# Optimization experiments

Measured on AMD Instinct MI355X. Metric: run time of the kernel, lower is better.

## Reference

```python
import jax, jax.numpy as jnp
import numpy as np

EPS = 1e-7
B, F, C, H, W, D = 2, 2, 64, 32, 104, 96


def _pix_homog(h, w):
    ys, xs = jnp.meshgrid(jnp.arange(h, dtype=jnp.float32),
                          jnp.arange(w, dtype=jnp.float32), indexing='ij')
    return jnp.stack([xs.ravel(), ys.ravel(), jnp.ones(h * w, jnp.float32)], 0)  # [3, H*W]


def setup_inputs() -> dict:
    key = jax.random.key(0)
    k1, k2 = jax.random.split(key)
    current_feats = jax.random.normal(k1, (B, C, H, W), jnp.float32)
    lookup_feats = jax.random.normal(k2, (B, F, C, H, W), jnp.float32)

    rng = np.random.RandomState(0)
    # intrinsics at matching (feature) resolution, monodepth2-style
    Km = np.eye(4, dtype=np.float32)
    Km[0, 0] = 0.58 * W
    Km[1, 1] = 1.92 * H
    Km[0, 2] = 0.5 * W
    Km[1, 2] = 0.5 * H
    K = np.tile(Km[None], (B, 1, 1))
    invK = np.linalg.inv(K).astype(np.float32)

    # near-identity relative poses (small rotation perturbation + small translation)
    poses = np.tile(np.eye(4, dtype=np.float32)[None, None], (B, F, 1, 1))
    poses[:, :, :3, :3] += 0.02 * rng.randn(B, F, 3, 3).astype(np.float32)
    poses[:, :, :3, 3] = 0.1 * rng.randn(B, F, 3).astype(np.float32)

    depth_bins = jnp.linspace(0.1, 20.0, D, dtype=jnp.float32)
    return {
        'current_feats': current_feats,
        'lookup_feats': lookup_feats,
        'poses': jnp.asarray(poses),
        'K': jnp.asarray(K),
        'invK': jnp.asarray(invK),
        'depth_bins': depth_bins,
    }


def _grid_sample_zeros(lfT, gx, gy, h, w):
    """Bilinear grid_sample, align_corners=True, padding_mode='zeros'.
    lfT: [B,F,H,W,C]; gx,gy: [B,F,D,H,W] in pixel coords. -> [B,F,D,H,W,C]"""
    x0 = jnp.floor(gx)
    y0 = jnp.floor(gy)
    x0i = x0.astype(jnp.int32)
    y0i = y0.astype(jnp.int32)
    wx1 = gx - x0
    wy1 = gy - y0
    wx0 = 1.0 - wx1
    wy0 = 1.0 - wy1
    bb = jnp.arange(lfT.shape[0])[:, None, None, None, None]
    ff = jnp.arange(lfT.shape[1])[None, :, None, None, None]

    def corner(yi, xi, wgt):
        m = ((xi >= 0) & (xi < w) & (yi >= 0) & (yi < h)).astype(lfT.dtype)
        xc = jnp.clip(xi, 0, w - 1)
        yc = jnp.clip(yi, 0, h - 1)
        v = lfT[bb, ff, yc, xc]                      # [B,F,D,H,W,C]
        return v * (m * wgt)[..., None]

    return (corner(y0i, x0i, wy0 * wx0) + corner(y0i, x0i + 1, wy0 * wx1)
            + corner(y0i + 1, x0i, wy1 * wx0) + corner(y0i + 1, x0i + 1, wy1 * wx1))


def reference(current_feats, lookup_feats, poses, K, invK, depth_bins):
    b, c, h, w = current_feats.shape
    f = lookup_feats.shape[1]
    d = depth_bins.shape[0]

    # Backproject: world points for each hypothesised depth plane
    pix = _pix_homog(h, w)                                   # [3, HW]
    cam = jnp.einsum('bij,jn->bin', invK[:, :3, :3], pix)    # [B,3,HW]
    pts = depth_bins[None, :, None, None] * cam[:, None]     # [B,D,3,HW]
    world = jnp.concatenate([pts, jnp.ones((b, d, 1, h * w), pts.dtype)], 2)  # [B,D,4,HW]

    # Project into each lookup frame
    P = jnp.einsum('bij,bfjk->bfik', K, poses)[:, :, :3, :]  # [B,F,3,4]
    cpts = jnp.einsum('bfij,bdjn->bfdin', P, world)          # [B,F,D,3,HW]
    xy = cpts[:, :, :, :2] / (cpts[:, :, :, 2:3] + EPS)      # pixel coords [B,F,D,2,HW]
    xy = xy.reshape(b, f, d, 2, h, w)
    gx, gy = xy[:, :, :, 0], xy[:, :, :, 1]                  # [B,F,D,H,W]

    # edge mask (detach in original -> stop_gradient)
    sx, sy = jax.lax.stop_gradient(gx), jax.lax.stop_gradient(gy)
    edge = ((sx >= 2.0) & (sx <= w - 2) & (sy >= 2.0) & (sy <= h - 2)).astype(jnp.float32)
    interior = jnp.zeros((h, w), jnp.float32).at[2:-2, 2:-2].set(1.0)
    edge_mask = edge * interior                               # [B,F,D,H,W]

    # warp lookup features and L1-diff against current features
    lfT = lookup_feats.transpose(0, 1, 3, 4, 2)               # [B,F,H,W,C]
    warped = _grid_sample_zeros(lfT, gx, gy, h, w)            # [B,F,D,H,W,C]
    cur = current_feats.transpose(0, 2, 3, 1)                 # [B,H,W,C]
    diffs = jnp.abs(warped - cur[:, None, None]).mean(-1) * edge_mask  # [B,F,D,H,W]

    # skip lookup frames whose pose is all-zero
    valid = (poses.sum((-2, -1)) != 0).astype(jnp.float32)    # [B,F]
    diffs = diffs * valid[:, :, None, None, None]

    cost = diffs.sum(1)                                        # [B,D,H,W]
    counts = (diffs > 0).astype(jnp.float32).sum(1)
    cost = cost / (counts + EPS)

    # set missing values to per-pixel max over depth bins
    missing = (cost == 0.0)
    cmax = cost.max(1, keepdims=True)
    cost = jnp.where(missing, cmax, cost)
    return cost
```

## Files before the change

### kernel.cpp

```cpp
#include <hip/hip_runtime.h>
#include <math.h>

constexpr int B_ = 2, F_ = 2, C_ = 64, H_ = 32, W_ = 104, D_ = 96;
constexpr int HW_ = H_ * W_;
#define EPSF 1e-7f

constexpr size_t LFP_ELEMS  = (size_t)B_ * F_ * HW_ * C_;
constexpr size_t CURT_OFF_F = LFP_ELEMS;

constexpr int NT_BLKS = (HW_ / 32) * (C_ / 32) * (B_ * F_ + B_);
constexpr int PXB   = 4;
constexpr int XT_   = W_ / PXB;
constexpr int DPAD  = D_ + 1;
constexpr int DPADI = D_ + 4;


template<int CTRL>
__device__ __forceinline__ float dpp_add(float x) {
    int y = __builtin_amdgcn_update_dpp(0, __float_as_int(x), CTRL, 0xf, 0xf, true);
    return x + __int_as_float(y);
}
__device__ __forceinline__ float group16_sum(float s) {
    s = dpp_add<0xB1>(s);
    s = dpp_add<0x4E>(s);
    s = dpp_add<0x141>(s);
    s = dpp_add<0x140>(s);
    return s;
}

__device__ __forceinline__ ushort f2bf(float f) {
    unsigned u = __float_as_uint(f);
    u += 0x7FFFu + ((u >> 16) & 1u);
    return (ushort)(u >> 16);
}

__device__ __forceinline__ float dot2bf(unsigned a, unsigned b, float acc) {
    float r;
    asm("v_dot2_f32_bf16 %0, %1, %2, %3" : "=v"(r) : "v"(a), "v"(b), "v"(acc));
    return r;
}

__global__ __launch_bounds__(256) void prep_kernel(
        const float* __restrict__ cur, const float* __restrict__ lf,
        float* __restrict__ ws) {
    __shared__ float tile[32][33];
    int bid = blockIdx.x;
    int slice = bid / 208;
    int rem   = bid % 208;
    int nb = rem % 104, cb = rem / 104;
    const float* inS = (slice < B_ * F_)
        ? lf  + (size_t)slice * C_ * HW_
        : cur + (size_t)(slice - B_ * F_) * C_ * HW_;
    int t = threadIdx.x;
    int tx = t & 31, ty = t >> 5;
    int n0 = nb * 32, c0 = cb * 32;
    int nx = (n0 + 32 < HW_) ? (n0 + 32) : (HW_ - 1);
    #pragma unroll
    for (int k = 0; k < 32; k += 8) {
        tile[ty + k][tx] = inS[(size_t)(c0 + ty + k) * HW_ + n0 + tx];
        if (tx == 0)
            tile[ty + k][32] = inS[(size_t)(c0 + ty + k) * HW_ + nx];
    }
    __syncthreads();
    if (slice < B_ * F_) {
        unsigned* outS = (unsigned*)ws + (size_t)slice * HW_ * C_;
        #pragma unroll
        for (int k = 0; k < 32; k += 8) {
            unsigned lo = f2bf(tile[tx][ty + k]);
            unsigned hi = f2bf(tile[tx][ty + k + 1]);
            outS[(size_t)(n0 + ty + k) * C_ + c0 + tx] = lo | (hi << 16);
        }
    } else {
        float* outS = ws + CURT_OFF_F + (size_t)(slice - B_ * F_) * HW_ * C_;
        #pragma unroll
        for (int k = 0; k < 32; k += 8)
            outS[(size_t)(n0 + ty + k) * C_ + c0 + tx] = tile[tx][ty + k];
    }
}

__global__ __launch_bounds__(256, 4) void mega_kernel(
        const float* __restrict__ poses, const float* __restrict__ K,
        const float* __restrict__ invK, const float* __restrict__ depth_bins,
        const float* __restrict__ ws, float* __restrict__ out) {
    int t   = threadIdx.x;
    int bid = blockIdx.x;
    int xt  = bid % XT_;  int r = bid / XT_;
    int y   = r % H_;
    int b   = r / H_;

    if (y < 2 || y >= H_ - 2) {
        for (int k = t; k < PXB * D_; k += 256) {
            int d = k >> 2, px = k & 3;
            out[((size_t)(b * D_ + d) * H_ + y) * W_ + xt * PXB + px] = 0.0f;
        }
        return;
    }

    __shared__ alignas(16) int offsL[F_][PXB][DPADI];
    __shared__ alignas(16) uint2 wtsL[F_][PXB][DPAD];
    __shared__ float  costb[PXB][DPAD];
    __shared__ float  pmax[32][PXB];
    __shared__ float  cmaxb[PXB];

    {
        int pxA = t & 3;
        int xA  = xt * PXB + pxA;
        const float* iK = invK + (size_t)b * 16;
        float xf = (float)xA, yf = (float)y;
        float cam0 = __fmul_rn(iK[0], xf); cam0 = __fmaf_rn(iK[1], yf, cam0); cam0 = __fmaf_rn(iK[2],  1.0f, cam0);
        float cam1 = __fmul_rn(iK[4], xf); cam1 = __fmaf_rn(iK[5], yf, cam1); cam1 = __fmaf_rn(iK[6],  1.0f, cam1);
        float cam2 = __fmul_rn(iK[8], xf); cam2 = __fmaf_rn(iK[9], yf, cam2); cam2 = __fmaf_rn(iK[10], 1.0f, cam2);
        bool interior = (xA >= 2) && (xA <= W_ - 3);

        #pragma unroll
        for (int f = 0; f < F_; ++f) {
            const float* Kb   = K + (size_t)b * 16;
            const float* pose = poses + (size_t)(b * F_ + f) * 16;
            float P[12];
            #pragma unroll
            for (int i = 0; i < 3; ++i) {
                #pragma unroll
                for (int k = 0; k < 4; ++k) {
                    float acc = __fmul_rn(Kb[i*4+0], pose[0*4+k]);
                    acc = __fmaf_rn(Kb[i*4+1], pose[1*4+k], acc);
                    acc = __fmaf_rn(Kb[i*4+2], pose[2*4+k], acc);
                    acc = __fmaf_rn(Kb[i*4+3], pose[3*4+k], acc);
                    P[i*4+k] = acc;
                }
            }
            float vs = 0.f;
            #pragma unroll
            for (int j = 0; j < 16; ++j) vs += pose[j];
            bool valid = (vs != 0.f);

            #pragma unroll
            for (int k = 0; k < 2; ++k) {
                int idx = t + 256 * k;
                if (idx < PXB * D_) {
                    int dd = idx >> 2;
                    float depth = depth_bins[dd];
                    float p0 = __fmul_rn(depth, cam0);
                    float p1 = __fmul_rn(depth, cam1);
                    float p2 = __fmul_rn(depth, cam2);
                    float c0 = __fmul_rn(P[0], p0); c0 = __fmaf_rn(P[1], p1, c0); c0 = __fmaf_rn(P[2],  p2, c0); c0 = __fmaf_rn(P[3],  1.0f, c0);
                    float c1 = __fmul_rn(P[4], p0); c1 = __fmaf_rn(P[5], p1, c1); c1 = __fmaf_rn(P[6],  p2, c1); c1 = __fmaf_rn(P[7],  1.0f, c1);
                    float c2 = __fmul_rn(P[8], p0); c2 = __fmaf_rn(P[9], p1, c2); c2 = __fmaf_rn(P[10], p2, c2); c2 = __fmaf_rn(P[11], 1.0f, c2);
                    float denom = __fadd_rn(c2, EPSF);
                    float gx = c0 / denom;
                    float gy = c1 / denom;
                    bool m = valid && interior && (gx >= 2.0f) && (gx <= (float)(W_ - 2))
                                               && (gy >= 2.0f) && (gy <= (float)(H_ - 2));
                    if (m) {
                        float x0f = floorf(gx), y0f = floorf(gy);
                        int   x0  = (int)x0f,   y0  = (int)y0f;
                        float wx1 = gx - x0f, wy1 = gy - y0f;
                        float wx0 = 1.f - wx1, wy0 = 1.f - wy1;
                        unsigned wlo = ((unsigned)f2bf(wy0 * wx1) << 16) | f2bf(wy0 * wx0);
                        unsigned whi = ((unsigned)f2bf(wy1 * wx1) << 16) | f2bf(wy1 * wx0);
                        wtsL[f][pxA][dd] = make_uint2(wlo, whi);
                        offsL[f][pxA][dd] = (y0 * W_ + x0) * C_;
                    } else {
                        offsL[f][pxA][dd] = -1;
                        wtsL[f][pxA][dd] = make_uint2(0u, 0u);
                    }
                }
            }
        }
    }
    __syncthreads();

    {
        int lane = t & 15, px = (t >> 4) & 3, half = t >> 6;
        int x = xt * PXB + px;
        const float4 cv = *(const float4*)(ws + CURT_OFF_F
                            + ((size_t)((b * H_ + y) * W_ + x)) * C_ + lane * 4);
        const unsigned* pfbase = (const unsigned*)ws;
        const unsigned* pf0a = pfbase + (size_t)(b * F_ + 0) * HW_ * C_ + lane * 4;
        const unsigned* pf0b = pf0a + W_ * C_;
        const unsigned* pf1a = pfbase + (size_t)(b * F_ + 1) * HW_ * C_ + lane * 4;
        const unsigned* pf1b = pf1a + W_ * C_;

        int dbeg = half * (D_ / 4);
        for (int ki4 = 0; ki4 < D_ / 16; ++ki4) {
            int dc4 = dbeg + ki4 * 4;
            int4 oq0 = *(const int4*)&offsL[0][px][dc4];
            int4 oq1 = *(const int4*)&offsL[1][px][dc4];
            int oa0[4] = {oq0.x, oq0.y, oq0.z, oq0.w};
            int oa1[4] = {oq1.x, oq1.y, oq1.z, oq1.w};

            #pragma unroll
            for (int jp = 0; jp < 2; ++jp) {
                uint4 q[2][4];
                #pragma unroll
                for (int u = 0; u < 2; ++u) {
                    int j = jp * 2 + u;
                    int oc0 = oa0[j], oc1 = oa1[j];
                    int os0 = oc0 & ~(oc0 >> 31);
                    int os1 = oc1 & ~(oc1 >> 31);
                    q[u][0] = *(const uint4*)(pf0a + os0);
                    q[u][1] = *(const uint4*)(pf0b + os0);
                    q[u][2] = *(const uint4*)(pf1a + os1);
                    q[u][3] = *(const uint4*)(pf1b + os1);
                }
                #pragma unroll
                for (int u = 0; u < 2; ++u) {
                    int j = jp * 2 + u;
                    int dc = dc4 + j;
                    uint2 w0 = wtsL[0][px][dc], w1 = wtsL[1][px][dc];
                    bool m0 = (oa0[j] >= 0), m1 = (oa1[j] >= 0);
                    uint4 A0 = q[u][0], B0 = q[u][1];
                    uint4 A1 = q[u][2], B1 = q[u][3];

                    float costsum = 0.f, counts = 0.f;
                    {
                        float s0 = dot2bf(B0.x, w0.y, dot2bf(A0.x, w0.x, -cv.x));
                        float s1 = dot2bf(B0.y, w0.y, dot2bf(A0.y, w0.x, -cv.y));
                        float s2 = dot2bf(B0.z, w0.y, dot2bf(A0.z, w0.x, -cv.z));
                        float s3 = dot2bf(B0.w, w0.y, dot2bf(A0.w, w0.x, -cv.w));
                        float s = (fabsf(s0) + fabsf(s1)) + (fabsf(s2) + fabsf(s3));
                        s = group16_sum(s);
                        float diff = __fmul_rn(s, 1.0f / 64.0f) * (m0 ? 1.0f : 0.0f);
                        costsum += diff;
                        counts  += (diff > 0.f) ? 1.0f : 0.0f;
                    }
                    {
                        float s0 = dot2bf(B1.x, w1.y, dot2bf(A1.x, w1.x, -cv.x));
                        float s1 = dot2bf(B1.y, w1.y, dot2bf(A1.y, w1.x, -cv.y));
                        float s2 = dot2bf(B1.z, w1.y, dot2bf(A1.z, w1.x, -cv.z));
                        float s3 = dot2bf(B1.w, w1.y, dot2bf(A1.w, w1.x, -cv.w));
                        float s = (fabsf(s0) + fabsf(s1)) + (fabsf(s2) + fabsf(s3));
                        s = group16_sum(s);
                        float diff = __fmul_rn(s, 1.0f / 64.0f) * (m1 ? 1.0f : 0.0f);
                        costsum += diff;
                        counts  += (diff > 0.f) ? 1.0f : 0.0f;
                    }
                    float cost = costsum * __builtin_amdgcn_rcpf(__fadd_rn(counts, EPSF));
                    if (lane == 0) costb[px][dc] = cost;
                }
            }
        }
    }
    __syncthreads();

    {
        int j = t >> 2, px = t & 3;
        float v[3];
        if (t < 128) {
            float pm = 0.f;
            #pragma unroll
            for (int k = 0; k < 3; ++k) {
                v[k] = costb[px][j + 32 * k];
                pm = fmaxf(pm, v[k]);
            }
            pmax[j][px] = pm;
        }
        __syncthreads();
        if (t < PXB) {
            float cm = 0.f;
            #pragma unroll
            for (int jj = 0; jj < 32; ++jj) cm = fmaxf(cm, pmax[jj][t]);
            cmaxb[t] = cm;
        }
        __syncthreads();
        if (t < 128) {
            float cm = cmaxb[px];
            int x = xt * PXB + px;
            #pragma unroll
            for (int k = 0; k < 3; ++k) {
                int d = j + 32 * k;
                out[((size_t)(b * D_ + d) * H_ + y) * W_ + x] = (v[k] == 0.0f) ? cm : v[k];
            }
        }
    }
}

extern "C" void kernel_launch(void* const* d_in, const int* in_sizes, int n_in,
                              void* d_out, int out_size, void* d_ws, size_t ws_size,
                              hipStream_t stream) {
    const float* cur        = (const float*)d_in[0];
    const float* lf         = (const float*)d_in[1];
    const float* poses      = (const float*)d_in[2];
    const float* K          = (const float*)d_in[3];
    const float* invK       = (const float*)d_in[4];
    const float* depth_bins = (const float*)d_in[5];
    float* out = (float*)d_out;
    float* ws  = (float*)d_ws;

    prep_kernel<<<NT_BLKS, 256, 0, stream>>>(cur, lf, ws);
    mega_kernel<<<B_ * H_ * XT_, 256, 0, stream>>>(poses, K, invK, depth_bins, ws, out);
}
```

Before: 96.39 us.

## Software-pipeline gather loads with double buffering and fold validity mask into weights

Restructures the per-depth gather loop into a double-buffered software pipeline, so the next depth's four feature loads are issued before the current depth's dot products run. Invalid samples now use offset 0 with a zero scale stored in a widened per-depth weight entry, which drops the sign-mask arithmetic and separate mask tests. A padding region of the offset table is zeroed so the final prefetch stays in bounds. The cost is twice the shared memory for weights and more live registers, which may lower occupancy.

```diff
diff --git a/kernel.cpp b/kernel.cpp
--- a/kernel.cpp
+++ b/kernel.cpp
@@ -97,12 +97,16 @@
     }
 
     __shared__ alignas(16) int offsL[F_][PXB][DPADI];
-    __shared__ alignas(16) uint2 wtsL[F_][PXB][DPAD];
+    __shared__ alignas(16) uint4 wtsL[F_][PXB][DPAD];
     __shared__ float  costb[PXB][DPAD];
     __shared__ float  pmax[32][PXB];
     __shared__ float  cmaxb[PXB];
 
     {
+        if (t < 32) {
+            int fp = t >> 4, pp = (t >> 2) & 3, kp = t & 3;
+            offsL[fp][pp][D_ + kp] = 0;
+        }
         int pxA = t & 3;
         int xA  = xt * PXB + pxA;
         const float* iK = invK + (size_t)b * 16;
@@ -157,11 +161,12 @@
                         float wx0 = 1.f - wx1, wy0 = 1.f - wy1;
                         unsigned wlo = ((unsigned)f2bf(wy0 * wx1) << 16) | f2bf(wy0 * wx0);
                         unsigned whi = ((unsigned)f2bf(wy1 * wx1) << 16) | f2bf(wy1 * wx0);
-                        wtsL[f][pxA][dd] = make_uint2(wlo, whi);
+                        wtsL[f][pxA][dd] = make_uint4(wlo, whi,
+                                                      __float_as_uint(1.0f / 64.0f), 0u);
                         offsL[f][pxA][dd] = (y0 * W_ + x0) * C_;
                     } else {
-                        offsL[f][pxA][dd] = -1;
-                        wtsL[f][pxA][dd] = make_uint2(0u, 0u);
+                        offsL[f][pxA][dd] = 0;
+                        wtsL[f][pxA][dd] = make_uint4(0u, 0u, 0u, 0u);
                     }
                 }
             }
@@ -180,65 +185,59 @@
         const unsigned* pf1a = pfbase + (size_t)(b * F_ + 1) * HW_ * C_ + lane * 4;
         const unsigned* pf1b = pf1a + W_ * C_;
 
+        #define ISSUE(dst, o0, o1) do {                       \
+            dst[0] = *(const uint4*)(pf0a + (o0));            \
+            dst[1] = *(const uint4*)(pf0b + (o0));            \
+            dst[2] = *(const uint4*)(pf1a + (o1));            \
+            dst[3] = *(const uint4*)(pf1b + (o1));            \
+        } while (0)
+
+        #define COMPUTE(dc, q) do {                                            \
+            uint4 w0 = wtsL[0][px][dc];                                        \
+            uint4 w1 = wtsL[1][px][dc];                                        \
+            float s0 = dot2bf(q[1].x, w0.y, dot2bf(q[0].x, w0.x, -cv.x));      \
+            float s1 = dot2bf(q[1].y, w0.y, dot2bf(q[0].y, w0.x, -cv.y));      \
+            float s2 = dot2bf(q[1].z, w0.y, dot2bf(q[0].z, w0.x, -cv.z));      \
+            float s3 = dot2bf(q[1].w, w0.y, dot2bf(q[0].w, w0.x, -cv.w));      \
+            float sA = (fabsf(s0) + fabsf(s1)) + (fabsf(s2) + fabsf(s3));      \
+            sA = group16_sum(sA);                                              \
+            float u0 = dot2bf(q[3].x, w1.y, dot2bf(q[2].x, w1.x, -cv.x));      \
+            float u1 = dot2bf(q[3].y, w1.y, dot2bf(q[2].y, w1.x, -cv.y));      \
+            float u2 = dot2bf(q[3].z, w1.y, dot2bf(q[2].z, w1.x, -cv.z));      \
+            float u3 = dot2bf(q[3].w, w1.y, dot2bf(q[2].w, w1.x, -cv.w));      \
+            float sB = (fabsf(u0) + fabsf(u1)) + (fabsf(u2) + fabsf(u3));      \
+            sB = group16_sum(sB);                                              \
+            float diff0 = __fmul_rn(sA, __uint_as_float(w0.z));                \
+            float diff1 = __fmul_rn(sB, __uint_as_float(w1.z));                \
+            float costsum = diff0 + diff1;                                     \
+            float counts = ((diff0 > 0.f) ? 1.0f : 0.0f)                       \
+                         + ((diff1 > 0.f) ? 1.0f : 0.0f);                      \
+            float cost = costsum * __builtin_amdgcn_rcpf(__fadd_rn(counts, EPSF)); \
+            if (lane == 0) costb[px][dc] = cost;                               \
+        } while (0)
+
         int dbeg = half * (D_ / 4);
-        for (int ki4 = 0; ki4 < D_ / 16; ++ki4) {
-            int dc4 = dbeg + ki4 * 4;
-            int4 oq0 = *(const int4*)&offsL[0][px][dc4];
-            int4 oq1 = *(const int4*)&offsL[1][px][dc4];
-            int oa0[4] = {oq0.x, oq0.y, oq0.z, oq0.w};
-            int oa1[4] = {oq1.x, oq1.y, oq1.z, oq1.w};
-
-            #pragma unroll
-            for (int jp = 0; jp < 2; ++jp) {
-                uint4 q[2][4];
-                #pragma unroll
-                for (int u = 0; u < 2; ++u) {
-                    int j = jp * 2 + u;
-                    int oc0 = oa0[j], oc1 = oa1[j];
-                    int os0 = oc0 & ~(oc0 >> 31);
-                    int os1 = oc1 & ~(oc1 >> 31);
-                    q[u][0] = *(const uint4*)(pf0a + os0);
-                    q[u][1] = *(const uint4*)(pf0b + os0);
-                    q[u][2] = *(const uint4*)(pf1a + os1);
-                    q[u][3] = *(const uint4*)(pf1b + os1);
-                }
-                #pragma unroll
-                for (int u = 0; u < 2; ++u) {
-                    int j = jp * 2 + u;
-                    int dc = dc4 + j;
-                    uint2 w0 = wtsL[0][px][dc], w1 = wtsL[1][px][dc];
-                    bool m0 = (oa0[j] >= 0), m1 = (oa1[j] >= 0);
-                    uint4 A0 = q[u][0], B0 = q[u][1];
-                    uint4 A1 = q[u][2], B1 = q[u][3];
-
-                    float costsum = 0.f, counts = 0.f;
-                    {
-                        float s0 = dot2bf(B0.x, w0.y, dot2bf(A0.x, w0.x, -cv.x));
-                        float s1 = dot2bf(B0.y, w0.y, dot2bf(A0.y, w0.x, -cv.y));
-                        float s2 = dot2bf(B0.z, w0.y, dot2bf(A0.z, w0.x, -cv.z));
-                        float s3 = dot2bf(B0.w, w0.y, dot2bf(A0.w, w0.x, -cv.w));
-                        float s = (fabsf(s0) + fabsf(s1)) + (fabsf(s2) + fabsf(s3));
-                        s = group16_sum(s);
-                        float diff = __fmul_rn(s, 1.0f / 64.0f) * (m0 ? 1.0f : 0.0f);
-                        costsum += diff;
-                        counts  += (diff > 0.f) ? 1.0f : 0.0f;
-                    }
-                    {
-                        float s0 = dot2bf(B1.x, w1.y, dot2bf(A1.x, w1.x, -cv.x));
-                        float s1 = dot2bf(B1.y, w1.y, dot2bf(A1.y, w1.x, -cv.y));
-                        float s2 = dot2bf(B1.z, w1.y, dot2bf(A1.z, w1.x, -cv.z));
-                        float s3 = dot2bf(B1.w, w1.y, dot2bf(A1.w, w1.x, -cv.w));
-                        float s = (fabsf(s0) + fabsf(s1)) + (fabsf(s2) + fabsf(s3));
-                        s = group16_sum(s);
-                        float diff = __fmul_rn(s, 1.0f / 64.0f) * (m1 ? 1.0f : 0.0f);
-                        costsum += diff;
-                        counts  += (diff > 0.f) ? 1.0f : 0.0f;
-                    }
-                    float cost = costsum * __builtin_amdgcn_rcpf(__fadd_rn(counts, EPSF));
-                    if (lane == 0) costb[px][dc] = cost;
-                }
-            }
-        }
+        int4 c0v = *(const int4*)&offsL[0][px][dbeg];
+        int4 c1v = *(const int4*)&offsL[1][px][dbeg];
+        uint4 qa[4], qb[4];
+        ISSUE(qa, c0v.x, c1v.x);
+
+        for (int g = 0; g < 6; ++g) {
+            int dc0 = dbeg + g * 4;
+            ISSUE(qb, c0v.y, c1v.y);
+            COMPUTE(dc0 + 0, qa);
+            ISSUE(qa, c0v.z, c1v.z);
+            COMPUTE(dc0 + 1, qb);
+            ISSUE(qb, c0v.w, c1v.w);
+            COMPUTE(dc0 + 2, qa);
+            c0v = *(const int4*)&offsL[0][px][dc0 + 4];
+            c1v = *(const int4*)&offsL[1][px][dc0 + 4];
+            ISSUE(qa, c0v.x, c1v.x);
+            COMPUTE(dc0 + 3, qb);
+        }
+
+        #undef ISSUE
+        #undef COMPUTE
     }
     __syncthreads();
 
```

After: 94.65 us (median of 2 runs). Within noise of the previous version (-1.8%).
